# Kernel optimization log

Hardware: AMD Instinct MI355X
Metric: run time of the kernel (lower is better)

## Reference

```python
import jax, jax.numpy as jnp
import numpy as np

NEG = -9.0e15

def gat_layer(X, adj_mask, W, Wb, a1, a2, ab):
    # X: [N, Fin]; W: [Fin, Fout]; a1,a2: [Fout]; ab: scalar
    h = X @ W + Wb                                   # [N, Fout]
    # a([h_i || h_j]) = h_i@a1 + h_j@a2 + ab  (decomposition of concat+linear)
    e = jax.nn.leaky_relu((h @ a1)[:, None] + (h @ a2)[None, :] + ab,
                          negative_slope=0.2)        # [N, N]
    e = jnp.where(adj_mask, e, NEG)
    attn = jax.nn.softmax(e, axis=1)                 # [N, N]
    return jax.nn.elu(attn @ h)                      # [N, Fout]

def setup_inputs() -> dict:
    key = jax.random.key(0)
    ks = jax.random.split(key, 12)
    N, Fin, Fh, H, Fout = 4096, 512, 128, 4, 64
    X = jax.random.normal(ks[0], (N, Fin), dtype=jnp.float32)
    adjacency_matrix = jax.random.randint(ks[1], (N, N), 0, 2, dtype=jnp.int32)
    s_in = 1.0 / np.sqrt(Fin)
    s_a = 1.0 / np.sqrt(2 * Fh)
    W_h  = jax.random.uniform(ks[2], (H, Fin, Fh), jnp.float32, -s_in, s_in)
    b_h  = jax.random.uniform(ks[3], (H, Fh), jnp.float32, -s_in, s_in)
    a1_h = jax.random.uniform(ks[4], (H, Fh), jnp.float32, -s_a, s_a)
    a2_h = jax.random.uniform(ks[5], (H, Fh), jnp.float32, -s_a, s_a)
    ab_h = jax.random.uniform(ks[6], (H,), jnp.float32, -s_a, s_a)
    Fcat = H * Fh
    s_c = 1.0 / np.sqrt(Fcat)
    s_ao = 1.0 / np.sqrt(2 * Fout)
    W_o  = jax.random.uniform(ks[7], (Fcat, Fout), jnp.float32, -s_c, s_c)
    b_o  = jax.random.uniform(ks[8], (Fout,), jnp.float32, -s_c, s_c)
    a1_o = jax.random.uniform(ks[9], (Fout,), jnp.float32, -s_ao, s_ao)
    a2_o = jax.random.uniform(ks[10], (Fout,), jnp.float32, -s_ao, s_ao)
    ab_o = jax.random.uniform(ks[11], (), jnp.float32, -s_ao, s_ao)
    return {"X": X, "adjacency_matrix": adjacency_matrix,
            "W_h": W_h, "b_h": b_h, "a1_h": a1_h, "a2_h": a2_h, "ab_h": ab_h,
            "W_o": W_o, "b_o": b_o, "a1_o": a1_o, "a2_o": a2_o, "ab_o": ab_o}

def reference(X, adjacency_matrix, W_h, b_h, a1_h, a2_h, ab_h,
              W_o, b_o, a1_o, a2_o, ab_o):
    adj_mask = adjacency_matrix > 0
    # per-head attention layers, vmapped over heads
    heads = jax.vmap(gat_layer, in_axes=(None, None, 0, 0, 0, 0, 0))(
        X, adj_mask, W_h, b_h, a1_h, a2_h, ab_h)      # [H, N, Fh]
    H, N, Fh = heads.shape
    x = jnp.transpose(heads, (1, 0, 2)).reshape(N, H * Fh)  # concat along features
    x = gat_layer(x, adj_mask, W_o, b_o, a1_o, a2_o, ab_o)  # [N, Fout]
    return jax.nn.log_softmax(x, axis=1)
```

## Files before the change

### kernel.cpp

```cpp
#include <hip/hip_runtime.h>
#include <math.h>

#define NN 4096
#define LOG2E 1.44269504088896340736f

using f32x2  = __attribute__((ext_vector_type(2))) float;
using f32x4  = __attribute__((ext_vector_type(4))) float;
using bf16x4 = __attribute__((ext_vector_type(4))) __bf16;
using bf16x8 = __attribute__((ext_vector_type(8))) __bf16;

#if __has_builtin(__builtin_amdgcn_exp2f)
#define EXP2(x) __builtin_amdgcn_exp2f(x)
#else
#define EXP2(x) __expf((x) * 0.6931471805599453f)
#endif

__device__ __forceinline__ void barrier_lgkm() {
    asm volatile("s_waitcnt lgkmcnt(0)\ns_barrier" ::: "memory");
}

template<int FH>
__device__ __forceinline__ void stage_tile(const __bf16* __restrict__ hgp,
                                           __bf16* dst, int tid) {
#pragma unroll
    for (int it = 0; it < FH / 32; it++) {
        int c = tid + it * 256;
        int f = c >> 3, sl = c & 7;
        int g = sl ^ (f & 7);
        __builtin_amdgcn_global_load_lds(
            (const __attribute__((address_space(1))) void*)(hgp + (size_t)f * NN + g * 8),
            (__attribute__((address_space(3))) void*)(dst + (size_t)c * 8), 16, 0, 0);
    }
}

__device__ __forceinline__ void stage_g(const __bf16* __restrict__ base, int ldk,
                                        __bf16* dst, int tid) {
#pragma unroll
    for (int it = 0; it < 2; it++) {
        int c = tid + it * 256;
        int f = c >> 3, sl = c & 7;
        int g = sl ^ (f & 7);
        __builtin_amdgcn_global_load_lds(
            (const __attribute__((address_space(1))) void*)(base + (size_t)f * ldk + g * 8),
            (__attribute__((address_space(3))) void*)(dst + (size_t)c * 8), 16, 0, 0);
    }
}

__global__ void pack_adj_kernel(const int* __restrict__ adj,
                                unsigned long long* __restrict__ bits) {
    int gw = (blockIdx.x * blockDim.x + threadIdx.x) >> 6;
    int lane = threadIdx.x & 63;
    int v = adj[(size_t)gw * 64 + lane];
    unsigned long long m = __ballot(v > 0);
    if (lane == 0) bits[gw] = m;
}

__global__ void prepack_kernel(const float* __restrict__ W_h, const float* __restrict__ b_h,
                               const float* __restrict__ W_o,
                               __bf16* __restrict__ Bt1, float* __restrict__ biasp,
                               __bf16* __restrict__ Bt2) {
    int idx = blockIdx.x * 256 + threadIdx.x;
    {
        int n = idx >> 9, k = idx & 511;
        int h = n >> 7, f = n & 127;
        Bt1[idx] = (__bf16)W_h[(size_t)h * 512 * 128 + k * 128 + f];
    }
    if (idx < 64 * 512) {
        int n = idx >> 9, k = idx & 511;
        Bt2[idx] = (__bf16)W_o[k * 64 + n];
    }
    if (idx < 512) biasp[idx] = b_h[idx];
}

__global__ void cast_bf16_kernel(const float* __restrict__ src, __bf16* __restrict__ dst) {
    int i = blockIdx.x * 256 + threadIdx.x;
    f32x4 v = *(const f32x4*)(src + (size_t)i * 4);
    bf16x4 o;
#pragma unroll
    for (int q = 0; q < 4; q++) o[q] = (__bf16)v[q];
    *(bf16x4*)(dst + (size_t)i * 4) = o;
}

__global__ __launch_bounds__(256) void gemm_fused_kernel(
    const __bf16* __restrict__ A, const __bf16* __restrict__ Bt,
    const float* __restrict__ bias,
    const float* __restrict__ a1, const float* __restrict__ a2,
    __bf16* __restrict__ Ht, float* __restrict__ s1, float* __restrict__ s2,
    int M, int N, int K)
{
    __shared__ __attribute__((aligned(16))) __bf16 As[2][64 * 64];
    __shared__ __attribute__((aligned(16))) __bf16 Bs[2][64 * 64];
    const int tid = threadIdx.x, w = tid >> 6, l = tid & 63, o = l >> 4, rl = l & 15;
    const int bm = blockIdx.y * 64, bn = blockIdx.x * 64;
    f32x4 acc[4] = {};
    stage_g(A + (size_t)bm * K, K, &As[0][0], tid);
    stage_g(Bt + (size_t)bn * K, K, &Bs[0][0], tid);
    const int KB = K / 64;
    for (int kb = 0; kb < KB; kb++) {
        int b = kb & 1;
        __syncthreads();
        if (kb + 1 < KB) {
            stage_g(A + (size_t)bm * K + (kb + 1) * 64, K, &As[b ^ 1][0], tid);
            stage_g(Bt + (size_t)bn * K + (kb + 1) * 64, K, &Bs[b ^ 1][0], tid);
        }
#pragma unroll
        for (int kt = 0; kt < 2; kt++) {
            int ra = w * 16 + rl;
            int cg = kt * 4 + o;
            bf16x8 af = *(const bf16x8*)(&As[b][(ra * 8 + (cg ^ (ra & 7))) * 8]);
#pragma unroll
            for (int nt = 0; nt < 4; nt++) {
                int rb = nt * 16 + rl;
                bf16x8 bfr = *(const bf16x8*)(&Bs[b][(rb * 8 + (cg ^ (rb & 7))) * 8]);
                acc[nt] = __builtin_amdgcn_mfma_f32_16x16x32_bf16(af, bfr, acc[nt], 0, 0, 0);
            }
        }
    }
    const int head = bn >> 7;
    const int row_base = bm + w * 16 + o * 4;
    float p1[4] = {0.f, 0.f, 0.f, 0.f}, p2[4] = {0.f, 0.f, 0.f, 0.f};
#pragma unroll
    for (int nt = 0; nt < 4; nt++) {
        int col = bn + nt * 16 + rl;
        float bv = bias[col];
        float a1v = a1[col] * LOG2E, a2v = a2[col] * LOG2E;
        bf16x4 hv;
#pragma unroll
        for (int r4 = 0; r4 < 4; r4++) {
            float h = acc[nt][r4] + bv;
            hv[r4] = (__bf16)h;
            p1[r4] += h * a1v;
            p2[r4] += h * a2v;
        }
        *(bf16x4*)(Ht + (size_t)col * M + row_base) = hv;
    }
#pragma unroll
    for (int r4 = 0; r4 < 4; r4++)
#pragma unroll
        for (int off = 1; off < 16; off <<= 1) {
            p1[r4] += __shfl_xor(p1[r4], off, 64);
            p2[r4] += __shfl_xor(p2[r4], off, 64);
        }
    if (rl == 0)
#pragma unroll
        for (int r4 = 0; r4 < 4; r4++) {
            atomicAdd(&s1[(size_t)head * M + row_base + r4], p1[r4]);
            atomicAdd(&s2[(size_t)head * M + row_base + r4], p2[r4]);
        }
}

__global__ void smax_kernel(const float* __restrict__ s2, float* __restrict__ s2max) {
    const float* p = s2 + (size_t)blockIdx.x * NN;
    int t = threadIdx.x;
    float m = -INFINITY;
    for (int i = t; i < NN; i += 256) m = fmaxf(m, p[i]);
#pragma unroll
    for (int off = 1; off < 64; off <<= 1) m = fmaxf(m, __shfl_xor(m, off, 64));
    __shared__ float red[4];
    if ((t & 63) == 0) red[t >> 6] = m;
    __syncthreads();
    if (t == 0) s2max[blockIdx.x] = fmaxf(fmaxf(red[0], red[1]), fmaxf(red[2], red[3]));
}

template<int FH, int JSPLIT>
__global__ __launch_bounds__(256, 4) void attn_kernel(
    const __bf16* __restrict__ Htg,
    const unsigned long long* __restrict__ adj_bits,
    const float* __restrict__ s1_all, const float* __restrict__ s2_all,
    const float* __restrict__ s2max_all, const float* __restrict__ ab_all,
    __bf16* __restrict__ accp,
    float* __restrict__ lg,
    int ldo)
{
    constexpr int NJT = NN / 64 / JSPLIT;
    constexpr int NTW = FH / 64;
    const int head = blockIdx.y;
    const int js   = blockIdx.z;
    const int row0 = blockIdx.x * 64;
    const int jt0  = js * NJT;
    const int tid = threadIdx.x;
    const int w = tid >> 6, l = tid & 63, o = l >> 4, rl = l & 15;
    const int myrow = row0 + w * 16 + rl;

    __shared__ __attribute__((aligned(16))) __bf16 hbuf[2][FH * 64];
    __shared__ __attribute__((aligned(16))) __bf16 plds[8 * 64 * 8];

    const float* s2 = s2_all + (size_t)head * NN;
    const __bf16* hg = Htg + (size_t)head * FH * NN;
    const float s1r = s1_all[(size_t)head * NN + myrow] + ab_all[head] * LOG2E;
    float mrow; { float x = s1r + s2max_all[head]; mrow = fmaxf(x, 0.2f * x); }
    float lacc = 0.f;
    f32x4 acc[4][NTW] = {};

    stage_tile<FH>(hg + (size_t)jt0 * 64, &hbuf[0][0], tid);

    auto produce = [&](int jt, bf16x8* fr) {
        unsigned long long aw = adj_bits[(size_t)myrow * 64 + jt];
#pragma unroll
        for (int kt = 0; kt < 2; kt++) {
            unsigned int mbyte = (unsigned int)(aw >> ((kt * 4 + o) * 8)) & 0xFFu;
            const float* sp = s2 + jt * 64 + kt * 32 + o * 8;
            f32x4 sa = *(const f32x4*)(sp);
            f32x4 sb = *(const f32x4*)(sp + 4);
            float ps = 0.f;
#pragma unroll
            for (int qp = 0; qp < 4; qp++) {
                f32x2 sv;
                sv[0] = (qp < 2) ? sa[qp * 2]     : sb[qp * 2 - 4];
                sv[1] = (qp < 2) ? sa[qp * 2 + 1] : sb[qp * 2 - 3];
                f32x2 x = sv + s1r;
                f32x2 e = __builtin_elementwise_max(x, 0.2f * x) - mrow;
#pragma unroll
                for (int h2 = 0; h2 < 2; h2++) {
                    int q = qp * 2 + h2;
                    float t = ((mbyte >> q) & 1u) ? e[h2] : -1.0e20f;
                    float p = EXP2(t);
                    fr[kt][q] = (__bf16)p;
                    ps += p;
                }
            }
            ps += __shfl_xor(ps, 16, 64);
            ps += __shfl_xor(ps, 32, 64);
            lacc += ps;
        }
    };

    bf16x8 freg[2];
    produce(jt0, freg);

    for (int jl = 0; jl < NJT; jl++) {
        const int b = jl & 1;
        const int jt = jt0 + jl;
#pragma unroll
        for (int kt = 0; kt < 2; kt++)
            *(bf16x8*)(&plds[((w * 2 + kt) * 64 + l) * 8]) = freg[kt];
        __syncthreads();
        if (jl + 1 < NJT)
            stage_tile<FH>(hg + (size_t)(jt + 1) * 64, &hbuf[b ^ 1][0], tid);
        bf16x8 bfr[2][NTW];
#pragma unroll
        for (int kt = 0; kt < 2; kt++)
#pragma unroll
            for (int ntl = 0; ntl < NTW; ntl++) {
                int f = (w * NTW + ntl) * 16 + rl;
                int slot = (kt * 4 + o) ^ (rl & 7);
                bfr[kt][ntl] = *(const bf16x8*)(&hbuf[b][(f * 8 + slot) * 8]);
            }
        bf16x8 fnext[2];
        if (jl + 1 < NJT) produce(jt + 1, fnext);
#pragma unroll
        for (int mt = 0; mt < 4; mt++)
#pragma unroll
            for (int kt = 0; kt < 2; kt++) {
                bf16x8 af = (mt == w) ? freg[kt]
                          : *(const bf16x8*)(&plds[((mt * 2 + kt) * 64 + l) * 8]);
#pragma unroll
                for (int ntl = 0; ntl < NTW; ntl++)
                    acc[mt][ntl] = __builtin_amdgcn_mfma_f32_16x16x32_bf16(
                        af, bfr[kt][ntl], acc[mt][ntl], 0, 0, 0);
            }
        barrier_lgkm();
        if (jl + 1 < NJT) { freg[0] = fnext[0]; freg[1] = fnext[1]; }
    }
    if (l < 16) lg[((size_t)head * JSPLIT + js) * NN + row0 + w * 16 + l] = lacc;
#pragma unroll
    for (int mt = 0; mt < 4; mt++)
#pragma unroll
        for (int ntl = 0; ntl < NTW; ntl++)
#pragma unroll
            for (int r4 = 0; r4 < 4; r4++) {
                int grow = row0 + mt * 16 + o * 4 + r4;
                int gcol = head * FH + (w * NTW + ntl) * 16 + rl;
                accp[((size_t)js * NN + grow) * ldo + gcol] = (__bf16)acc[mt][ntl][r4];
            }
}

__global__ void combine1_kernel(const __bf16* __restrict__ accp, const float* __restrict__ lg,
                                __bf16* __restrict__ outb) {
    int gid = blockIdx.x * 256 + threadIdx.x;
    int row = gid >> 7, c4 = (gid & 127) * 4;
    int head = c4 >> 7;
    float lsum = 0.f;
#pragma unroll
    for (int js = 0; js < 4; js++) lsum += lg[((size_t)head * 4 + js) * NN + row];
    float inv = lsum > 0.f ? 1.f / lsum : 0.f;
    float v[4] = {0.f, 0.f, 0.f, 0.f};
#pragma unroll
    for (int js = 0; js < 4; js++) {
        bf16x4 t = *(const bf16x4*)(accp + ((size_t)js * NN + row) * 512 + c4);
#pragma unroll
        for (int q = 0; q < 4; q++) v[q] += (float)t[q];
    }
    bf16x4 ob;
#pragma unroll
    for (int q = 0; q < 4; q++) {
        float x = v[q] * inv;
        x = x > 0.f ? x : __expf(x) - 1.f;
        ob[q] = (__bf16)x;
    }
    *(bf16x4*)(outb + (size_t)row * 512 + c4) = ob;
}

__global__ void combine2_kernel(const __bf16* __restrict__ accp, const float* __restrict__ lg,
                                float* __restrict__ out) {
    int row = (blockIdx.x * 256 + threadIdx.x) >> 6;
    int lane = threadIdx.x & 63;
    if (row >= NN) return;
    float lsum = 0.f, v = 0.f;
#pragma unroll
    for (int js = 0; js < 16; js++) {
        lsum += lg[(size_t)js * NN + row];
        v += (float)accp[((size_t)js * NN + row) * 64 + lane];
    }
    float inv = lsum > 0.f ? 1.f / lsum : 0.f;
    v *= inv;
    v = v > 0.f ? v : __expf(v) - 1.f;
    float m = v;
#pragma unroll
    for (int off = 1; off < 64; off <<= 1) m = fmaxf(m, __shfl_xor(m, off, 64));
    float ex = __expf(v - m);
    float s = ex;
#pragma unroll
    for (int off = 1; off < 64; off <<= 1) s += __shfl_xor(s, off, 64);
    out[(size_t)row * 64 + lane] = v - m - __logf(s);
}

extern "C" void kernel_launch(void* const* d_in, const int* in_sizes, int n_in,
                              void* d_out, int out_size, void* d_ws, size_t ws_size,
                              hipStream_t stream) {
    const float* X    = (const float*)d_in[0];
    const int*   adj  = (const int*)d_in[1];
    const float* W_h  = (const float*)d_in[2];
    const float* b_h  = (const float*)d_in[3];
    const float* a1_h = (const float*)d_in[4];
    const float* a2_h = (const float*)d_in[5];
    const float* ab_h = (const float*)d_in[6];
    const float* W_o  = (const float*)d_in[7];
    const float* b_o  = (const float*)d_in[8];
    const float* a1_o = (const float*)d_in[9];
    const float* a2_o = (const float*)d_in[10];
    const float* ab_o = (const float*)d_in[11];
    float* out = (float*)d_out;

    char* ws = (char*)d_ws;
    auto alloc = [&](size_t bytes) {
        char* p = ws; ws += (bytes + 255) & ~(size_t)255; return p;
    };
    unsigned long long* adj_bits = (unsigned long long*)alloc((size_t)NN * 64 * 8);
    __bf16* Bt1    = (__bf16*)alloc((size_t)512 * 512 * 2);
    float*  biasp  = (float*)alloc(512 * 4);
    __bf16* Bt2    = (__bf16*)alloc((size_t)64 * 512 * 2);
    __bf16* Xb     = (__bf16*)alloc((size_t)NN * 512 * 2);
    float*  s1h    = (float*)alloc((size_t)4 * NN * 4);
    float*  s2h    = (float*)alloc((size_t)4 * NN * 4);
    float*  s1o    = (float*)alloc((size_t)NN * 4);
    float*  s2o    = (float*)alloc((size_t)NN * 4);
    float*  s2maxh = (float*)alloc(4 * 4);
    float*  s2maxo = (float*)alloc(4);
    __bf16* Htg    = (__bf16*)alloc((size_t)512 * NN * 2);
    __bf16* accp1  = (__bf16*)alloc((size_t)4 * NN * 512 * 2);
    float*  lg1    = (float*)alloc((size_t)16 * NN * 4);
    __bf16* outhb  = (__bf16*)alloc((size_t)NN * 512 * 2);
    __bf16* Ht2    = (__bf16*)alloc((size_t)64 * NN * 2);
    __bf16* accp2  = (__bf16*)alloc((size_t)16 * NN * 64 * 2);
    float*  lg2    = (float*)alloc((size_t)16 * NN * 4);

    hipMemsetAsync(s1h, 0, (size_t)(4 + 4 + 1 + 1) * NN * 4, stream);
    pack_adj_kernel<<<(NN * 64) / 4, 256, 0, stream>>>(adj, adj_bits);
    prepack_kernel<<<1024, 256, 0, stream>>>(W_h, b_h, W_o, Bt1, biasp, Bt2);
    cast_bf16_kernel<<<(NN * 512 / 4) / 256, 256, 0, stream>>>(X, Xb);
    gemm_fused_kernel<<<dim3(8, 64), 256, 0, stream>>>(
        Xb, Bt1, biasp, a1_h, a2_h, Htg, s1h, s2h, NN, 512, 512);
    smax_kernel<<<4, 256, 0, stream>>>(s2h, s2maxh);
    attn_kernel<128, 4><<<dim3(NN / 64, 4, 4), 256, 0, stream>>>(
        Htg, adj_bits, s1h, s2h, s2maxh, ab_h, accp1, lg1, 512);
    combine1_kernel<<<(NN * 128) / 256, 256, 0, stream>>>(accp1, lg1, outhb);
    gemm_fused_kernel<<<dim3(1, 64), 256, 0, stream>>>(
        outhb, Bt2, b_o, a1_o, a2_o, Ht2, s1o, s2o, NN, 64, 512);
    smax_kernel<<<1, 256, 0, stream>>>(s2o, s2maxo);
    attn_kernel<64, 16><<<dim3(NN / 64, 1, 16), 256, 0, stream>>>(
        Ht2, adj_bits, s1o, s2o, s2maxo, ab_o, accp2, lg2, 64);
    combine2_kernel<<<(NN * 64) / 256, 256, 0, stream>>>(accp2, lg2, out);
}
```

Baseline: 228.0 us.

## Prefetch adjacency/score loads two tiles ahead, stagger tile order, simplify leaky-relu math

Splits the probability producer into a load phase and a math phase so the adjacency and s2 global loads are issued two tiles ahead, hiding their latency behind MFMA work. Blocks start the column-tile loop at a rotated offset so blocks do not hit the same H tiles at the same time. The leaky-relu is folded into two FMAs plus a max, the row-sum shuffles move out of the loop to a single reduction at the end, and MFMA sections run at raised wave priority. It costs extra registers for the prefetched data, which may reduce occupancy.

Result: slower. 270.3 us (+18.5%).

```diff
diff --git a/kernel.cpp b/kernel.cpp
--- a/kernel.cpp
+++ b/kernel.cpp
@@ -181,6 +181,7 @@
     const int tid = threadIdx.x;
     const int w = tid >> 6, l = tid & 63, o = l >> 4, rl = l & 15;
     const int myrow = row0 + w * 16 + rl;
+    const int off = blockIdx.x & (NJT - 1);
 
     __shared__ __attribute__((aligned(16))) __bf16 hbuf[2][FH * 64];
     __shared__ __attribute__((aligned(16))) __bf16 plds[8 * 64 * 8];
@@ -189,54 +190,59 @@
     const __bf16* hg = Htg + (size_t)head * FH * NN;
     const float s1r = s1_all[(size_t)head * NN + myrow] + ab_all[head] * LOG2E;
     float mrow; { float x = s1r + s2max_all[head]; mrow = fmaxf(x, 0.2f * x); }
+    const float u0 = s1r - mrow;
+    const float v0 = fmaf(0.2f, s1r, -mrow);
     float lacc = 0.f;
     f32x4 acc[4][NTW] = {};
 
-    stage_tile<FH>(hg + (size_t)jt0 * 64, &hbuf[0][0], tid);
-
-    auto produce = [&](int jt, bf16x8* fr) {
-        unsigned long long aw = adj_bits[(size_t)myrow * 64 + jt];
+    auto ring = [&](int i) { return jt0 + ((i + off) & (NJT - 1)); };
+
+    struct PLoad { unsigned long long aw; f32x4 sa[2]; f32x4 sb[2]; };
+    auto pload = [&](int jt) {
+        PLoad L;
+        L.aw = adj_bits[(size_t)myrow * 64 + jt];
 #pragma unroll
         for (int kt = 0; kt < 2; kt++) {
-            unsigned int mbyte = (unsigned int)(aw >> ((kt * 4 + o) * 8)) & 0xFFu;
             const float* sp = s2 + jt * 64 + kt * 32 + o * 8;
-            f32x4 sa = *(const f32x4*)(sp);
-            f32x4 sb = *(const f32x4*)(sp + 4);
+            L.sa[kt] = *(const f32x4*)(sp);
+            L.sb[kt] = *(const f32x4*)(sp + 4);
+        }
+        return L;
+    };
+    auto pmath = [&](const PLoad& L, bf16x8* fr) {
+#pragma unroll
+        for (int kt = 0; kt < 2; kt++) {
+            unsigned int mbyte = (unsigned int)(L.aw >> ((kt * 4 + o) * 8)) & 0xFFu;
             float ps = 0.f;
 #pragma unroll
-            for (int qp = 0; qp < 4; qp++) {
-                f32x2 sv;
-                sv[0] = (qp < 2) ? sa[qp * 2]     : sb[qp * 2 - 4];
-                sv[1] = (qp < 2) ? sa[qp * 2 + 1] : sb[qp * 2 - 3];
-                f32x2 x = sv + s1r;
-                f32x2 e = __builtin_elementwise_max(x, 0.2f * x) - mrow;
-#pragma unroll
-                for (int h2 = 0; h2 < 2; h2++) {
-                    int q = qp * 2 + h2;
-                    float t = ((mbyte >> q) & 1u) ? e[h2] : -1.0e20f;
-                    float p = EXP2(t);
-                    fr[kt][q] = (__bf16)p;
-                    ps += p;
-                }
-            }
-            ps += __shfl_xor(ps, 16, 64);
-            ps += __shfl_xor(ps, 32, 64);
+            for (int q = 0; q < 8; q++) {
+                float s = (q < 4) ? L.sa[kt][q] : L.sb[kt][q - 4];
+                float u = s + u0;
+                float v = fmaf(0.2f, s, v0);
+                float t = fmaxf(u, v);
+                t = ((mbyte >> q) & 1u) ? t : -1.0e20f;
+                float p = EXP2(t);
+                fr[kt][q] = (__bf16)p;
+                ps += p;
+            }
             lacc += ps;
         }
     };
 
+    stage_tile<FH>(hg + (size_t)ring(0) * 64, &hbuf[0][0], tid);
+    PLoad L = pload(ring(0));
     bf16x8 freg[2];
-    produce(jt0, freg);
+    pmath(L, freg);
+    if (NJT > 1) L = pload(ring(1));
 
     for (int jl = 0; jl < NJT; jl++) {
         const int b = jl & 1;
-        const int jt = jt0 + jl;
 #pragma unroll
         for (int kt = 0; kt < 2; kt++)
             *(bf16x8*)(&plds[((w * 2 + kt) * 64 + l) * 8]) = freg[kt];
         __syncthreads();
         if (jl + 1 < NJT)
-            stage_tile<FH>(hg + (size_t)(jt + 1) * 64, &hbuf[b ^ 1][0], tid);
+            stage_tile<FH>(hg + (size_t)ring(jl + 1) * 64, &hbuf[b ^ 1][0], tid);
         bf16x8 bfr[2][NTW];
 #pragma unroll
         for (int kt = 0; kt < 2; kt++)
@@ -247,7 +253,9 @@
                 bfr[kt][ntl] = *(const bf16x8*)(&hbuf[b][(f * 8 + slot) * 8]);
             }
         bf16x8 fnext[2];
-        if (jl + 1 < NJT) produce(jt + 1, fnext);
+        if (jl + 1 < NJT) pmath(L, fnext);
+        if (jl + 2 < NJT) L = pload(ring(jl + 2));
+        __builtin_amdgcn_s_setprio(1);
 #pragma unroll
         for (int mt = 0; mt < 4; mt++)
 #pragma unroll
@@ -259,9 +267,12 @@
                     acc[mt][ntl] = __builtin_amdgcn_mfma_f32_16x16x32_bf16(
                         af, bfr[kt][ntl], acc[mt][ntl], 0, 0, 0);
             }
+        __builtin_amdgcn_s_setprio(0);
         barrier_lgkm();
         if (jl + 1 < NJT) { freg[0] = fnext[0]; freg[1] = fnext[1]; }
     }
+    lacc += __shfl_xor(lacc, 16, 64);
+    lacc += __shfl_xor(lacc, 32, 64);
     if (l < 16) lg[((size_t)head * JSPLIT + js) * NN + row0 + w * 16 + l] = lacc;
 #pragma unroll
     for (int mt = 0; mt < 4; mt++)
```
